# Optimization experiments

Hardware: AMD Instinct MI355X
Metric: run time of the kernel (lower is better)

The kernel has to match this reference:

```python
import jax, jax.numpy as jnp
import numpy as np

IN_CH = 1024   # backbone channels
N_T = 81       # n_targets (COCO classes + bg)
K = 7          # PSROI grid size
H = 100        # feature map height
WID = 100      # feature map width
R = 1024       # number of regions
S = 2          # bilinear sampling points per bin edge (PSROIAlign-style average)


def setup_inputs() -> dict:
    key = jax.random.key(0)
    k1, k2, k3 = jax.random.split(key, 3)
    x = jax.random.normal(k1, (IN_CH, H, WID), dtype=jnp.float32)
    # regions: fractional (i, j, h, w) = (center_y, center_x, height, width) in [0,1]
    regions = jax.random.uniform(k2, (R, 4), dtype=jnp.float32)
    conv_w = jax.random.normal(k3, (N_T * K * K, IN_CH), dtype=jnp.float32) * 0.02
    conv_b = jnp.zeros((N_T * K * K,), dtype=jnp.float32)
    return {"x": x, "regions": regions, "conv_w": conv_w, "conv_b": conv_b}


def _bilinear_pool(map_thw, ys, xs):
    """Average of bilinear samples of one bin's score map.

    map_thw: (T, H, W) score map for this (u, v) bin's channel group.
    ys: (R, S) sample row coords.  xs: (R, S) sample col coords.
    Returns (R, T): per-region average-pooled bin value.
    """
    Hm, Wm = map_thw.shape[1], map_thw.shape[2]
    ys = jnp.clip(ys, 0.0, Hm - 1)
    xs = jnp.clip(xs, 0.0, Wm - 1)
    y0 = jnp.floor(ys)
    x0 = jnp.floor(xs)
    y0i = y0.astype(jnp.int32)
    x0i = x0.astype(jnp.int32)
    y1i = jnp.minimum(y0i + 1, Hm - 1)
    x1i = jnp.minimum(x0i + 1, Wm - 1)
    wy1 = ys - y0
    wy0 = 1.0 - wy1
    wx1 = xs - x0
    wx0 = 1.0 - wx1

    def g(yi, xi):  # gather (T, R, S, S)
        return map_thw[:, yi[:, :, None], xi[:, None, :]]

    v = (g(y0i, x0i) * (wy0[:, :, None] * wx0[:, None, :])
         + g(y0i, x1i) * (wy0[:, :, None] * wx1[:, None, :])
         + g(y1i, x0i) * (wy1[:, :, None] * wx0[:, None, :])
         + g(y1i, x1i) * (wy1[:, :, None] * wx1[:, None, :]))
    return v.mean((2, 3)).T  # (R, T)


def reference(x, regions, conv_w, conv_b):
    # 1x1 conv score map: (n_targets*k^2, H, W)
    sm = jnp.einsum('oc,chw->ohw', conv_w, x) + conv_b[:, None, None]
    sm = sm.reshape(N_T, K, K, H, WID)  # (T, ky, kx, H, W) position-sensitive groups

    # region geometry (fractional center/size -> absolute feature-map coords)
    top = (regions[:, 0] - regions[:, 2] * 0.5) * H     # (R,)
    left = (regions[:, 1] - regions[:, 3] * 0.5) * WID  # (R,)
    bh = regions[:, 2] * H / K                          # bin height
    bw = regions[:, 3] * WID / K                        # bin width

    off = (jnp.arange(S, dtype=jnp.float32) + 0.5) / S  # (S,) sample offsets in bin
    bins = jnp.arange(K, dtype=jnp.float32)             # (K,)
    ys = top[:, None, None] + (bins[None, :, None] + off[None, None, :]) * bh[:, None, None]   # (R,K,S)
    xs = left[:, None, None] + (bins[None, :, None] + off[None, None, :]) * bw[:, None, None]  # (R,K,S)

    # vmap over the k x k position-sensitive bins; bin (u,v) reads channel group (:,u,v)
    inner = jax.vmap(_bilinear_pool, in_axes=(1, None, 1))  # over kx: sm axis, xs axis
    outer = jax.vmap(inner, in_axes=(1, 1, None))           # over ky: sm axis, ys axis
    pooled = outer(sm, ys, xs)  # (K, K, R, T)

    # pooled.mean(-1).mean(-1) over the k x k grid
    scores = pooled.mean((0, 1))  # (R, T)
    return scores
```

## Files before the change

### kernel.cpp

```cpp
#include <hip/hip_runtime.h>
#include <cstddef>

#define IN_CH 1024
#define NT    81
#define KGRID 7
#define NBINS 49
#define HH    100
#define WW    100
#define NPIX  (HH*WW)
#define NREG  1024
#define COLB  82
#define NCOL  (NBINS*COLB)
#define NPADW 4096
#define SBIN  84
#define SROWB (NBINS*SBIN)
#define NG    8
#define NSC   2560
#define PXB   ((NPIX + 31) / 32)
#define PXG   (PXB * (IN_CH / 128))
#define PREPG (PXG + NPADW)

#define GM_T  40
#define GN_T  16
#define NKT   16

typedef unsigned short ushortT;
typedef short bf16x8 __attribute__((ext_vector_type(8)));
typedef float f32x4  __attribute__((ext_vector_type(4)));

static __device__ __forceinline__ unsigned short f2bf(float f) {
    unsigned int u = __builtin_bit_cast(unsigned int, f);
    return (unsigned short)((u + 0x7fffu + ((u >> 16) & 1u)) >> 16);
}

static __device__ __forceinline__ void gld_lds16(const ushortT* g, ushortT* l) {
    __builtin_amdgcn_global_load_lds(
        (__attribute__((address_space(1))) void*)(unsigned long long)(uintptr_t)g,
        (__attribute__((address_space(3))) void*)(unsigned int)(unsigned long long)(uintptr_t)l,
        16, 0, 0);
}

static __device__ __forceinline__ void barf() {
    asm volatile("" ::: "memory");
    __builtin_amdgcn_s_barrier();
    asm volatile("" ::: "memory");
}

__global__ __launch_bounds__(256) void prep_fused(const float* __restrict__ x,
                                                  ushortT* __restrict__ xbT,
                                                  const float* __restrict__ conv_w,
                                                  ushortT* __restrict__ Wr) {
    __shared__ float tile[128][33];
    const int tid = threadIdx.x;
    const int bid = blockIdx.x;
    if (bid < PXG) {
        const int p0 = (bid % PXB) * 32;
        const int c0 = (bid / PXB) * 128;
        const int pl = tid & 31;
        const int cg = tid >> 5;
        const int p = p0 + pl;
#pragma unroll
        for (int it = 0; it < 16; ++it) {
            const int c = it * 8 + cg;
            tile[c][pl] = (p < NPIX) ? x[(size_t)(c0 + c) * NPIX + p] : 0.0f;
        }
        __syncthreads();
#pragma unroll
        for (int pass = 0; pass < 2; ++pass) {
            const int pix = pass * 16 + (tid >> 4);
            const int cb  = (tid & 15) * 8;
            if (p0 + pix < NPIX) {
                uint4 pk;
                pk.x = (unsigned int)f2bf(tile[cb + 0][pix]) | ((unsigned int)f2bf(tile[cb + 1][pix]) << 16);
                pk.y = (unsigned int)f2bf(tile[cb + 2][pix]) | ((unsigned int)f2bf(tile[cb + 3][pix]) << 16);
                pk.z = (unsigned int)f2bf(tile[cb + 4][pix]) | ((unsigned int)f2bf(tile[cb + 5][pix]) << 16);
                pk.w = (unsigned int)f2bf(tile[cb + 6][pix]) | ((unsigned int)f2bf(tile[cb + 7][pix]) << 16);
                *(uint4*)(xbT + (size_t)(p0 + pix) * IN_CH + c0 + cb) = pk;
            }
        }
    } else {
        const int row = bid - PXG;
        const int bin = row / COLB;
        const int t   = row - bin * COLB;
        const int c   = tid * 4;
        uint2 pk; pk.x = 0; pk.y = 0;
        if (bin < NBINS && t < NT) {
            const float4 v = *(const float4*)(conv_w + ((size_t)(t * NBINS + bin)) * IN_CH + c);
            pk.x = (unsigned int)f2bf(v.x) | ((unsigned int)f2bf(v.y) << 16);
            pk.y = (unsigned int)f2bf(v.z) | ((unsigned int)f2bf(v.w) << 16);
        }
        *(uint2*)(Wr + (size_t)row * IN_CH + c) = pk;
    }
}

__global__ __launch_bounds__(512, 2) void gemm_sm(const ushortT* __restrict__ xbT,
                                                  const ushortT* __restrict__ Wr,
                                                  unsigned char* __restrict__ sm,
                                                  float* __restrict__ scales) {
    __shared__ ushortT lA[2][16384];
    __shared__ ushortT lB[2][16384];

    const int tid  = threadIdx.x;
    const int lane = tid & 63;
    const int w    = tid >> 6;
    const int wm   = w & 1;
    const int wn   = w >> 1;

    const int bid   = blockIdx.x;
    const int sw    = (bid & 7) * 80 + (bid >> 3);
    const int mtile = sw >> 4;
    const int ntile = sw & 15;
    const int p0 = mtile * 256;
    const int n0 = ntile * 256;

    const int l3   = lane >> 3;
    const int srco = ((lane & 7) ^ l3) << 3;
    const int w2   = w * 2;

    const ushortT* gA[2][2];
    const ushortT* gB[2][2];
    int dstA[2][2];
#pragma unroll
    for (int h = 0; h < 2; ++h)
#pragma unroll
        for (int it = 0; it < 2; ++it) {
            const int hr = (w2 + it) * 8 + l3;
            int p = p0 + h * 128 + hr; if (p > NPIX - 1) p = NPIX - 1;
            gA[h][it] = xbT + (size_t)p * IN_CH + srco;
            gB[h][it] = Wr + (size_t)(n0 + h * 128 + hr) * IN_CH + srco;
            dstA[h][it] = h * 8192 + (w2 + it) * 512 + lane * 8;
        }

#define STAGE_A(bb, h, T) { gld_lds16(gA[h][0] + (size_t)(T) * 64, &lA[bb][dstA[h][0]]); \
                            gld_lds16(gA[h][1] + (size_t)(T) * 64, &lA[bb][dstA[h][1]]); }
#define STAGE_B(bb, h, T) { gld_lds16(gB[h][0] + (size_t)(T) * 64, &lB[bb][dstA[h][0]]); \
                            gld_lds16(gB[h][1] + (size_t)(T) * 64, &lB[bb][dstA[h][1]]); }

    const int m_l = lane & 15;
    const int kq  = lane >> 4;
    const int ph0 = ((kq) ^ (lane & 7)) << 3;
    const int ph1 = ((4 + kq) ^ (lane & 7)) << 3;
    const int arow = (wm * 128 + m_l) * 64;
    const int brow = (wn * 64 + m_l) * 64;

#define RD_A(bb, mq) { _Pragma("unroll") for (int mt = 0; mt < 4; ++mt) { \
        const int ro = arow + ((mq) * 64 + mt * 16) * 64; \
        af[mt][0] = *(const bf16x8*)(&lA[bb][ro + ph0]); \
        af[mt][1] = *(const bf16x8*)(&lA[bb][ro + ph1]); } }
#define RD_B(dst, bb, nq) { _Pragma("unroll") for (int nt = 0; nt < 2; ++nt) { \
        const int ro = brow + ((nq) * 32 + nt * 16) * 64; \
        dst[nt][0] = *(const bf16x8*)(&lB[bb][ro + ph0]); \
        dst[nt][1] = *(const bf16x8*)(&lB[bb][ro + ph1]); } }
#define MM(mq, B, nq) { _Pragma("unroll") for (int mt = 0; mt < 4; ++mt) \
        _Pragma("unroll") for (int nt = 0; nt < 2; ++nt) { \
        acc[mq][mt][nq][nt] = __builtin_amdgcn_mfma_f32_16x16x32_bf16(af[mt][0], B[nt][0], acc[mq][mt][nq][nt], 0, 0, 0); \
        acc[mq][mt][nq][nt] = __builtin_amdgcn_mfma_f32_16x16x32_bf16(af[mt][1], B[nt][1], acc[mq][mt][nq][nt], 0, 0, 0); } }

    f32x4 acc[2][4][2][2];
#pragma unroll
    for (int a = 0; a < 2; ++a)
#pragma unroll
        for (int b = 0; b < 4; ++b)
#pragma unroll
            for (int c = 0; c < 2; ++c)
#pragma unroll
                for (int d = 0; d < 2; ++d) acc[a][b][c][d] = (f32x4){0.f, 0.f, 0.f, 0.f};

    bf16x8 af[4][2], bf0[2][2], bf1[2][2];

    STAGE_A(0, 0, 0); STAGE_A(0, 1, 0); STAGE_B(0, 0, 0); STAGE_B(0, 1, 0);
    STAGE_A(1, 0, 1); STAGE_A(1, 1, 1); STAGE_B(1, 0, 1); STAGE_B(1, 1, 1);
    asm volatile("s_waitcnt vmcnt(8)" ::: "memory");
    __builtin_amdgcn_s_barrier();
    asm volatile("" ::: "memory");

#pragma unroll 2
    for (int kt = 0; kt < NKT; ++kt) {
        const int b = kt & 1;
        RD_A(b, 0);
        RD_B(bf0, b, 0);
        RD_B(bf1, b, 1);
        __builtin_amdgcn_s_setprio(1);
        MM(0, bf0, 0);
        __builtin_amdgcn_s_setprio(0);
        __builtin_amdgcn_s_setprio(1);
        MM(0, bf1, 1);
        __builtin_amdgcn_s_setprio(0);
        barf();
        RD_A(b, 1);
        if (kt < NKT - 2) { STAGE_B(b, 0, kt + 2); STAGE_B(b, 1, kt + 2); }
        __builtin_amdgcn_s_setprio(1);
        MM(1, bf1, 1);
        __builtin_amdgcn_s_setprio(0);
        barf();
        __builtin_amdgcn_s_setprio(1);
        MM(1, bf0, 0);
        __builtin_amdgcn_s_setprio(0);
        if (kt < NKT - 2) {
            STAGE_A(b, 0, kt + 2); STAGE_A(b, 1, kt + 2);
            asm volatile("s_waitcnt vmcnt(8)" ::: "memory");
        } else {
            asm volatile("s_waitcnt vmcnt(0)" ::: "memory");
        }
        __builtin_amdgcn_s_barrier();
        asm volatile("" ::: "memory");
    }

    __syncthreads();
    float am = 0.0f;
#pragma unroll
    for (int mq = 0; mq < 2; ++mq)
#pragma unroll
        for (int mt = 0; mt < 4; ++mt)
#pragma unroll
            for (int nq = 0; nq < 2; ++nq)
#pragma unroll
                for (int nt = 0; nt < 2; ++nt)
#pragma unroll
                    for (int rg = 0; rg < 4; ++rg)
                        am = fmaxf(am, fabsf(acc[mq][mt][nq][nt][rg]));
#pragma unroll
    for (int off = 32; off > 0; off >>= 1) am = fmaxf(am, __shfl_xor(am, off));
    float* red = (float*)lA;
    if (lane == 0) red[w] = am;
    __syncthreads();
    const float qam = fmaxf(fmaxf(red[w], red[w ^ 2]), 1e-30f);
    const float inv = 127.0f / qam;
    if (lane == 0 && (wn & 1) == 0)
        scales[(mtile * 2 + wm) * 32 + ntile * 2 + (wn >> 1)] = qam * (1.0f / 127.0f);

    const int prow0 = p0 + wm * 128 + kq * 4;
    const int ncol0 = n0 + wn * 64 + m_l;
    int  coloff[2][2];
    bool cok[2][2];
#pragma unroll
    for (int nq = 0; nq < 2; ++nq)
#pragma unroll
        for (int nt = 0; nt < 2; ++nt) {
            const int n = ncol0 + nq * 32 + nt * 16;
            cok[nq][nt] = (n < NCOL);
            coloff[nq][nt] = n + 2 * (n / COLB);
        }
#pragma unroll
    for (int mq = 0; mq < 2; ++mq)
#pragma unroll
        for (int mt = 0; mt < 4; ++mt)
#pragma unroll
            for (int rg = 0; rg < 4; ++rg) {
                const int p = prow0 + mq * 64 + mt * 16 + rg;
                if (p < NPIX) {
                    unsigned char* rowp = sm + (size_t)p * SROWB;
#pragma unroll
                    for (int nq = 0; nq < 2; ++nq)
#pragma unroll
                        for (int nt = 0; nt < 2; ++nt)
                            if (cok[nq][nt]) {
                                const int q = __float2int_rn(acc[mq][mt][nq][nt][rg] * inv);
                                rowp[coloff[nq][nt]] = (unsigned char)(signed char)q;
                            }
                }
            }
#undef STAGE_A
#undef STAGE_B
#undef RD_A
#undef RD_B
#undef MM
}

__global__ __launch_bounds__(256) void pool_kernel(const unsigned char* __restrict__ sm,
                                                   const float* __restrict__ scales,
                                                   const float* __restrict__ regions,
                                                   const float* __restrict__ conv_b,
                                                   float* __restrict__ out) {
    __shared__ int   rowo[28]; __shared__ float roww[28];
    __shared__ int   coli[28]; __shared__ float colw[28];
    __shared__ int   pofs[120];
    __shared__ float pw[120];
    __shared__ int   pptb[120];
    __shared__ int   pnb[120];
    __shared__ float part[40][100];
    const int tid = threadIdx.x;
    const int r = blockIdx.x;
    const int g = blockIdx.y;

    if (tid < 28) {
        const float4 reg = *(const float4*)(regions + (size_t)r * 4);
        const float top = (reg.x - reg.z * 0.5f) * (float)HH;
        const float bh  = reg.z * ((float)HH / (float)KGRID);
        const int u = tid >> 2, i = tid & 3;
        const int s = i >> 1, hi = i & 1;
        float y = top + ((float)u + ((float)s + 0.5f) * 0.5f) * bh;
        y = fminf(fmaxf(y, 0.0f), (float)(HH - 1));
        const float y0f = floorf(y);
        const int y0 = (int)y0f;
        const float wy1 = y - y0f;
        rowo[tid] = (hi ? min(y0 + 1, HH - 1) : y0) * WW;
        roww[tid] = hi ? wy1 : (1.0f - wy1);
    } else if (tid >= 32 && tid < 60) {
        const float4 reg = *(const float4*)(regions + (size_t)r * 4);
        const float left = (reg.y - reg.w * 0.5f) * (float)WW;
        const float bw   = reg.w * ((float)WW / (float)KGRID);
        const int idx = tid - 32;
        const int v = idx >> 2, j = idx & 3;
        const int s = j >> 1, hi = j & 1;
        float xx = left + ((float)v + ((float)s + 0.5f) * 0.5f) * bw;
        xx = fminf(fmaxf(xx, 0.0f), (float)(WW - 1));
        const float x0f = floorf(xx);
        const int x0 = (int)x0f;
        const float wx1 = xx - x0f;
        coli[idx] = hi ? min(x0 + 1, WW - 1) : x0;
        colw[idx] = hi ? wx1 : (1.0f - wx1);
    }
    __syncthreads();
    if (tid < 120) {
        if (tid < 98) {
            const int tt = g * 98 + tid;
            const int bin = tt >> 4, tap = tt & 15;
            const int u = bin / KGRID, v = bin - u * KGRID;
            const int i = tap >> 2, j = tap & 3;
            const int pix = rowo[u * 4 + i] + coli[v * 4 + j];
            pofs[tid] = pix * SROWB + bin * SBIN;
            pw[tid]   = roww[u * 4 + i] * colw[v * 4 + j] * (1.0f / 196.0f);
            pptb[tid] = (pix >> 7) * 32;
            pnb[tid]  = bin * COLB;
        } else {
            pofs[tid] = 0;
            pw[tid]   = 0.0f;
            pptb[tid] = 0;
            pnb[tid]  = 0;
        }
    }
    __syncthreads();

    const int lane = tid & 63, w = tid >> 6;
    const int sub  = lane / 6;
    const int cg   = lane - sub * 6;
    if (sub < 10) {
        const int str = w * 10 + sub;
        uint4 v[3];
#pragma unroll
        for (int it = 0; it < 3; ++it)
            v[it] = *(const uint4*)(sm + pofs[it * 40 + str] + cg * 16);

        float acc[16];
#pragma unroll
        for (int ch = 0; ch < 16; ++ch) acc[ch] = 0.0f;
#pragma unroll
        for (int it = 0; it < 3; ++it) {
            const int l  = it * 40 + str;
            const float wt = pw[l];
            const int nb  = pnb[l] + cg * 16;
            const int nt0 = nb >> 7;
            const int rr  = nb & 127;
            const float s0 = scales[pptb[l] + nt0];
            const float s1 = scales[pptb[l] + nt0 + 1];
            const float w0 = wt * s0, w1 = wt * s1;
            const unsigned int uu[4] = {v[it].x, v[it].y, v[it].z, v[it].w};
#pragma unroll
            for (int b = 0; b < 4; ++b) {
#pragma unroll
                for (int k = 0; k < 4; ++k) {
                    const int ch = b * 4 + k;
                    const int q = (int)(signed char)((uu[b] >> (k * 8)) & 0xff);
                    acc[ch] += ((rr < 128 - ch) ? w0 : w1) * (float)q;
                }
            }
        }
#pragma unroll
        for (int b = 0; b < 4; ++b) {
            float4 p4;
            p4.x = acc[b * 4]; p4.y = acc[b * 4 + 1];
            p4.z = acc[b * 4 + 2]; p4.w = acc[b * 4 + 3];
            *(float4*)&part[str][cg * 16 + b * 4] = p4;
        }
    }
    __syncthreads();
    if (tid < NT) {
        float vv = 0.f;
#pragma unroll
        for (int s = 0; s < 40; ++s) vv += part[s][tid];
        if (g == 0) {
            float bsum = 0.f;
            for (int bin = 0; bin < NBINS; ++bin) bsum += conv_b[tid * NBINS + bin];
            vv += bsum * (1.0f / (float)NBINS);
        }
        atomicAdd(out + (size_t)r * NT + tid, vv);
    }
}

__global__ __launch_bounds__(256) void xpose_kernel(const float* __restrict__ x,
                                                    float* __restrict__ xt) {
    __shared__ float tile[32][33];
    const int p0 = blockIdx.x * 32;
    const int c0 = blockIdx.y * 32;
    const int tx = threadIdx.x;
    const int ty = threadIdx.y;
#pragma unroll
    for (int k = 0; k < 32; k += 8) {
        const int p = p0 + tx;
        if (p < NPIX) tile[ty + k][tx] = x[(size_t)(c0 + ty + k) * NPIX + p];
    }
    __syncthreads();
#pragma unroll
    for (int k = 0; k < 32; k += 8) {
        const int p = p0 + ty + k;
        if (p < NPIX) xt[(size_t)p * IN_CH + (c0 + tx)] = tile[tx][ty + k];
    }
}

template <bool XPOSED>
__global__ __launch_bounds__(256) void psroi_kernel(
    const float* __restrict__ xsrc, const float* __restrict__ regions,
    const float* __restrict__ conv_w, const float* __restrict__ conv_b,
    float* __restrict__ out) {
    __shared__ float w_lds[32 * 96];
    __shared__ float g_lds[32 * 64];
    __shared__ int   rowoff[64][4];
    __shared__ float rowwf[64][4];
    __shared__ int   colidx[64][4];
    __shared__ float colwf[64][4];
    const int tid = threadIdx.x;
    const int bin = blockIdx.x >> 4;
    const int rg  = blockIdx.x & 15;
    const int u = bin / KGRID, v = bin % KGRID;
    const int r0 = rg * 64;
    if (tid < 64) {
        const float4 reg = *(const float4*)(regions + (size_t)(r0 + tid) * 4);
        const float top  = (reg.x - reg.z * 0.5f) * (float)HH;
        const float left = (reg.y - reg.w * 0.5f) * (float)WW;
        const float bh = reg.z * ((float)HH / (float)KGRID);
        const float bw = reg.w * ((float)WW / (float)KGRID);
        const float scale = 1.0f / 196.0f;
#pragma unroll
        for (int s = 0; s < 2; s++) {
            const float off = (s + 0.5f) * 0.5f;
            float yy = top + ((float)u + off) * bh;
            yy = fminf(fmaxf(yy, 0.0f), (float)(HH - 1));
            const float y0f = floorf(yy);
            const int y0 = (int)y0f;
            const float wy1 = yy - y0f;
            rowoff[tid][2 * s] = y0 * WW;
            rowoff[tid][2 * s + 1] = min(y0 + 1, HH - 1) * WW;
            rowwf[tid][2 * s] = (1.0f - wy1) * scale;
            rowwf[tid][2 * s + 1] = wy1 * scale;
            float xx = left + ((float)v + off) * bw;
            xx = fminf(fmaxf(xx, 0.0f), (float)(WW - 1));
            const float x0f = floorf(xx);
            const int x0 = (int)x0f;
            const float wx1 = xx - x0f;
            colidx[tid][2 * s] = x0;
            colidx[tid][2 * s + 1] = min(x0 + 1, WW - 1);
            colwf[tid][2 * s] = 1.0f - wx1;
            colwf[tid][2 * s + 1] = wx1;
        }
    }
    const int ri = tid & 15, tq = tid >> 4, rb = tid >> 2, cq = tid & 3;
    float acc[4][6];
#pragma unroll
    for (int m = 0; m < 4; m++)
#pragma unroll
        for (int k = 0; k < 6; k++) acc[m][k] = 0.0f;
    for (int chunk = 0; chunk < IN_CH / 32; chunk++) {
        const int c0 = chunk * 32;
        __syncthreads();
#pragma unroll
        for (int it = 0; it < 12; it++) {
            const int idx = it * 256 + tid;
            const int t = idx >> 5, c = idx & 31;
            float val = 0.0f;
            if (t < NT) val = conv_w[(size_t)(t * NBINS + bin) * IN_CH + c0 + c];
            w_lds[c * 96 + t] = val;
        }
        const int cbase = c0 + cq * 8;
        float g8[8];
#pragma unroll
        for (int cc = 0; cc < 8; cc++) g8[cc] = 0.0f;
#pragma unroll
        for (int i = 0; i < 4; i++) {
            const int ro = rowoff[rb][i];
            const float wy = rowwf[rb][i];
#pragma unroll
            for (int j = 0; j < 4; j++) {
                const int pix = ro + colidx[rb][j];
                const float wv = wy * colwf[rb][j];
                if (XPOSED) {
                    const float4* p = (const float4*)(xsrc + (size_t)pix * IN_CH + cbase);
                    const float4 a = p[0]; const float4 b = p[1];
                    g8[0] += wv * a.x; g8[1] += wv * a.y; g8[2] += wv * a.z; g8[3] += wv * a.w;
                    g8[4] += wv * b.x; g8[5] += wv * b.y; g8[6] += wv * b.z; g8[7] += wv * b.w;
                } else {
#pragma unroll
                    for (int cc = 0; cc < 8; cc++)
                        g8[cc] += wv * xsrc[(size_t)(cbase + cc) * NPIX + pix];
                }
            }
        }
#pragma unroll
        for (int cc = 0; cc < 8; cc++) g_lds[(cq * 8 + cc) * 64 + rb] = g8[cc];
        __syncthreads();
#pragma unroll 4
        for (int c = 0; c < 32; c++) {
            float wv[6];
#pragma unroll
            for (int k = 0; k < 6; k++) wv[k] = w_lds[c * 96 + tq * 6 + k];
            const float4 gq = *(const float4*)&g_lds[c * 64 + ri * 4];
            const float gm[4] = {gq.x, gq.y, gq.z, gq.w};
#pragma unroll
            for (int m = 0; m < 4; m++)
#pragma unroll
                for (int k = 0; k < 6; k++) acc[m][k] += gm[m] * wv[k];
        }
    }
    const float invK2 = 1.0f / 49.0f;
#pragma unroll
    for (int k = 0; k < 6; k++) {
        const int t = tq * 6 + k;
        if (t < NT) {
            const float bterm = conv_b[t * NBINS + bin] * invK2;
#pragma unroll
            for (int m = 0; m < 4; m++) {
                const int rr = r0 + ri * 4 + m;
                atomicAdd(&out[(size_t)rr * NT + t], acc[m][k] + bterm);
            }
        }
    }
}

extern "C" void kernel_launch(void* const* d_in, const int* in_sizes, int n_in,
                              void* d_out, int out_size, void* d_ws, size_t ws_size,
                              hipStream_t stream) {
    const float* x       = (const float*)d_in[0];
    const float* regions = (const float*)d_in[1];
    const float* conv_w  = (const float*)d_in[2];
    const float* conv_b  = (const float*)d_in[3];
    float* out = (float*)d_out;

    const size_t sz_xbT = (size_t)NPIX * IN_CH * 2;
    const size_t sz_Wr  = (size_t)NPADW * IN_CH * 2;
    const size_t sz_sm  = (size_t)NPIX * SROWB + 256;
    const size_t sz_sc  = (size_t)NSC * sizeof(float);
    const size_t need   = sz_xbT + sz_Wr + sz_sm + sz_sc;

    if (ws_size >= need) {
        ushortT* xbT = (ushortT*)d_ws;
        ushortT* Wr  = (ushortT*)((char*)d_ws + sz_xbT);
        unsigned char* sm = (unsigned char*)d_ws + sz_xbT + sz_Wr;
        float* scales = (float*)((char*)d_ws + sz_xbT + sz_Wr + sz_sm);
        hipMemsetAsync(out, 0, (size_t)out_size * sizeof(float), stream);
        prep_fused<<<dim3(PREPG), 256, 0, stream>>>(x, xbT, conv_w, Wr);
        gemm_sm<<<dim3(GM_T * GN_T), 512, 0, stream>>>(xbT, Wr, sm, scales);
        pool_kernel<<<dim3(NREG, NG), 256, 0, stream>>>(sm, scales, regions, conv_b, out);
    } else {
        hipMemsetAsync(out, 0, (size_t)out_size * sizeof(float), stream);
        const size_t xt_bytes = (size_t)NPIX * IN_CH * sizeof(float);
        const dim3 mainGrid(NBINS * 16);
        if (ws_size >= xt_bytes) {
            float* xt = (float*)d_ws;
            xpose_kernel<<<dim3((NPIX + 31) / 32, IN_CH / 32), dim3(32, 8), 0, stream>>>(x, xt);
            psroi_kernel<true><<<mainGrid, 256, 0, stream>>>(xt, regions, conv_w, conv_b, out);
        } else {
            psroi_kernel<false><<<mainGrid, 256, 0, stream>>>(x, regions, conv_w, conv_b, out);
        }
    }
}
```

Before: 228.9 us.

## Process all bins per region in one pool block, drop atomics and memset

```diff
diff --git a/kernel.cpp b/kernel.cpp
--- a/kernel.cpp
+++ b/kernel.cpp
@@ -14,11 +14,10 @@
 #define NPADW 4096
 #define SBIN  84
 #define SROWB (NBINS*SBIN)
-#define NG    8
 #define NSC   2560
 #define PXB   ((NPIX + 31) / 32)
 #define PXG   (PXB * (IN_CH / 128))
-#define PREPG (PXG + NPADW)
+#define PREPG (PXG + NPADW / 8)
 
 #define GM_T  40
 #define GN_T  16
@@ -79,17 +78,21 @@
             }
         }
     } else {
-        const int row = bid - PXG;
-        const int bin = row / COLB;
-        const int t   = row - bin * COLB;
-        const int c   = tid * 4;
-        uint2 pk; pk.x = 0; pk.y = 0;
-        if (bin < NBINS && t < NT) {
-            const float4 v = *(const float4*)(conv_w + ((size_t)(t * NBINS + bin)) * IN_CH + c);
-            pk.x = (unsigned int)f2bf(v.x) | ((unsigned int)f2bf(v.y) << 16);
-            pk.y = (unsigned int)f2bf(v.z) | ((unsigned int)f2bf(v.w) << 16);
-        }
-        *(uint2*)(Wr + (size_t)row * IN_CH + c) = pk;
+        const int row0 = (bid - PXG) * 8;
+        const int c    = tid * 4;
+#pragma unroll
+        for (int rr = 0; rr < 8; ++rr) {
+            const int row = row0 + rr;
+            const int bin = row / COLB;
+            const int t   = row - bin * COLB;
+            uint2 pk; pk.x = 0; pk.y = 0;
+            if (bin < NBINS && t < NT) {
+                const float4 v = *(const float4*)(conv_w + ((size_t)(t * NBINS + bin)) * IN_CH + c);
+                pk.x = (unsigned int)f2bf(v.x) | ((unsigned int)f2bf(v.y) << 16);
+                pk.y = (unsigned int)f2bf(v.z) | ((unsigned int)f2bf(v.w) << 16);
+            }
+            *(uint2*)(Wr + (size_t)row * IN_CH + c) = pk;
+        }
     }
 }
 
@@ -274,14 +277,13 @@
                                                    float* __restrict__ out) {
     __shared__ int   rowo[28]; __shared__ float roww[28];
     __shared__ int   coli[28]; __shared__ float colw[28];
-    __shared__ int   pofs[120];
-    __shared__ float pw[120];
-    __shared__ int   pptb[120];
-    __shared__ int   pnb[120];
+    __shared__ int   pofs[800];
+    __shared__ float pw[800];
+    __shared__ int   pptb[800];
+    __shared__ int   pnb[800];
     __shared__ float part[40][100];
     const int tid = threadIdx.x;
     const int r = blockIdx.x;
-    const int g = blockIdx.y;
 
     if (tid < 28) {
         const float4 reg = *(const float4*)(regions + (size_t)r * 4);
@@ -312,22 +314,25 @@
         colw[idx] = hi ? wx1 : (1.0f - wx1);
     }
     __syncthreads();
-    if (tid < 120) {
-        if (tid < 98) {
-            const int tt = g * 98 + tid;
-            const int bin = tt >> 4, tap = tt & 15;
-            const int u = bin / KGRID, v = bin - u * KGRID;
-            const int i = tap >> 2, j = tap & 3;
-            const int pix = rowo[u * 4 + i] + coli[v * 4 + j];
-            pofs[tid] = pix * SROWB + bin * SBIN;
-            pw[tid]   = roww[u * 4 + i] * colw[v * 4 + j] * (1.0f / 196.0f);
-            pptb[tid] = (pix >> 7) * 32;
-            pnb[tid]  = bin * COLB;
-        } else {
-            pofs[tid] = 0;
-            pw[tid]   = 0.0f;
-            pptb[tid] = 0;
-            pnb[tid]  = 0;
+#pragma unroll
+    for (int base = 0; base < 800; base += 256) {
+        const int idx = base + tid;
+        if (idx < 800) {
+            if (idx < 784) {
+                const int bin = idx >> 4, tap = idx & 15;
+                const int u = bin / KGRID, v = bin - u * KGRID;
+                const int i = tap >> 2, j = tap & 3;
+                const int pix = rowo[u * 4 + i] + coli[v * 4 + j];
+                pofs[idx] = pix * SROWB + bin * SBIN;
+                pw[idx]   = roww[u * 4 + i] * colw[v * 4 + j] * (1.0f / 196.0f);
+                pptb[idx] = (pix >> 7) * 32;
+                pnb[idx]  = bin * COLB;
+            } else {
+                pofs[idx] = 0;
+                pw[idx]   = 0.0f;
+                pptb[idx] = 0;
+                pnb[idx]  = 0;
+            }
         }
     }
     __syncthreads();
@@ -337,34 +342,45 @@
     const int cg   = lane - sub * 6;
     if (sub < 10) {
         const int str = w * 10 + sub;
-        uint4 v[3];
-#pragma unroll
-        for (int it = 0; it < 3; ++it)
+
+        float acc[16];
+#pragma unroll
+        for (int ch = 0; ch < 16; ++ch) acc[ch] = 0.0f;
+
+        uint4 v[4], vn[4];
+#pragma unroll
+        for (int it = 0; it < 4; ++it)
             v[it] = *(const uint4*)(sm + pofs[it * 40 + str] + cg * 16);
 
-        float acc[16];
-#pragma unroll
-        for (int ch = 0; ch < 16; ++ch) acc[ch] = 0.0f;
-#pragma unroll
-        for (int it = 0; it < 3; ++it) {
-            const int l  = it * 40 + str;
-            const float wt = pw[l];
-            const int nb  = pnb[l] + cg * 16;
-            const int nt0 = nb >> 7;
-            const int rr  = nb & 127;
-            const float s0 = scales[pptb[l] + nt0];
-            const float s1 = scales[pptb[l] + nt0 + 1];
-            const float w0 = wt * s0, w1 = wt * s1;
-            const unsigned int uu[4] = {v[it].x, v[it].y, v[it].z, v[it].w};
-#pragma unroll
-            for (int b = 0; b < 4; ++b) {
-#pragma unroll
-                for (int k = 0; k < 4; ++k) {
-                    const int ch = b * 4 + k;
-                    const int q = (int)(signed char)((uu[b] >> (k * 8)) & 0xff);
-                    acc[ch] += ((rr < 128 - ch) ? w0 : w1) * (float)q;
+        for (int gp = 0; gp < 5; ++gp) {
+            if (gp < 4) {
+#pragma unroll
+                for (int it = 0; it < 4; ++it)
+                    vn[it] = *(const uint4*)(sm + pofs[(gp * 4 + 4 + it) * 40 + str] + cg * 16);
+            }
+#pragma unroll
+            for (int it = 0; it < 4; ++it) {
+                const int l  = (gp * 4 + it) * 40 + str;
+                const float wt = pw[l];
+                const int nb  = pnb[l] + cg * 16;
+                const int nt0 = nb >> 7;
+                const int rr  = nb & 127;
+                const float s0 = scales[pptb[l] + nt0];
+                const float s1 = scales[pptb[l] + nt0 + 1];
+                const float w0 = wt * s0, w1 = wt * s1;
+                const unsigned int uu[4] = {v[it].x, v[it].y, v[it].z, v[it].w};
+#pragma unroll
+                for (int b = 0; b < 4; ++b) {
+#pragma unroll
+                    for (int k = 0; k < 4; ++k) {
+                        const int ch = b * 4 + k;
+                        const int q = (int)(signed char)((uu[b] >> (k * 8)) & 0xff);
+                        acc[ch] += ((rr < 128 - ch) ? w0 : w1) * (float)q;
+                    }
                 }
             }
+#pragma unroll
+            for (int it = 0; it < 4; ++it) v[it] = vn[it];
         }
 #pragma unroll
         for (int b = 0; b < 4; ++b) {
@@ -379,12 +395,9 @@
         float vv = 0.f;
 #pragma unroll
         for (int s = 0; s < 40; ++s) vv += part[s][tid];
-        if (g == 0) {
-            float bsum = 0.f;
-            for (int bin = 0; bin < NBINS; ++bin) bsum += conv_b[tid * NBINS + bin];
-            vv += bsum * (1.0f / (float)NBINS);
-        }
-        atomicAdd(out + (size_t)r * NT + tid, vv);
+        float bsum = 0.f;
+        for (int bin = 0; bin < NBINS; ++bin) bsum += conv_b[tid * NBINS + bin];
+        out[(size_t)r * NT + tid] = vv + bsum * (1.0f / (float)NBINS);
     }
 }
 
@@ -546,10 +559,9 @@
         ushortT* Wr  = (ushortT*)((char*)d_ws + sz_xbT);
         unsigned char* sm = (unsigned char*)d_ws + sz_xbT + sz_Wr;
         float* scales = (float*)((char*)d_ws + sz_xbT + sz_Wr + sz_sm);
-        hipMemsetAsync(out, 0, (size_t)out_size * sizeof(float), stream);
         prep_fused<<<dim3(PREPG), 256, 0, stream>>>(x, xbT, conv_w, Wr);
         gemm_sm<<<dim3(GM_T * GN_T), 512, 0, stream>>>(xbT, Wr, sm, scales);
-        pool_kernel<<<dim3(NREG, NG), 256, 0, stream>>>(sm, scales, regions, conv_b, out);
+        pool_kernel<<<dim3(NREG), 256, 0, stream>>>(sm, scales, regions, conv_b, out);
     } else {
         hipMemsetAsync(out, 0, (size_t)out_size * sizeof(float), stream);
         const size_t xt_bytes = (size_t)NPIX * IN_CH * sizeof(float);
```

Result: no change. 228.3 us (-0.2%).
